# Performance work log

Measured on AMD Instinct MI355X. Metric: run time of the kernel, lower is better.

The kernel has to match this reference:

```python
import jax, jax.numpy as jnp
import numpy as np

B = 4; S_L = 512; WIN = 256; SCH = 3; CCH = 128; F = 8; P = 4; RNN = 128; FC = 256
L1 = (WIN - F + 1) // P          # after conv1 + pool1
L2 = (L1 - F + 1) // P           # after conv2 + pool2
D1 = L2 * CCH                    # flattened conv feature dim fed to GRU


def _conv1d(x, w, b):
    # x: (N, W, Cin), w: (F, Cin, Cout), VALID, stride 1 (matches keras Conv1D)
    return jax.lax.conv_general_dilated(x, w, (1,), 'VALID', dimension_numbers=('NWC', 'WIO', 'NWC')) + b


def _maxpool(x, p):
    return jax.lax.reduce_window(x, -jnp.inf, jax.lax.max, (1, p, 1), (1, p, 1), 'VALID')


def _gru(x, h0, mask, W, U, b):
    # keras GRU v2 (reset_after=True). b[0]=input bias, b[1]=recurrent bias.
    # Masked steps carry state through (keras semantics: output==state for GRU).
    u = U.shape[0]
    xg = x @ W + b[0]  # (B, T, 3u) precomputed input projections
    br = b[1]

    def step(h, inp):
        xt, mt = inp  # (B, 3u), (B,)
        rg = h @ U + br
        z = jax.nn.sigmoid(xt[:, :u] + rg[:, :u])
        r = jax.nn.sigmoid(xt[:, u:2 * u] + rg[:, u:2 * u])
        hh = jnp.tanh(xt[:, 2 * u:] + r * rg[:, 2 * u:])
        hn = z * h + (1.0 - z) * hh
        hn = jnp.where(mt[:, None], hn, h)
        return hn, hn

    _, ys = jax.lax.scan(step, h0, (jnp.swapaxes(xg, 0, 1), jnp.swapaxes(mask, 0, 1)))
    return jnp.swapaxes(ys, 0, 1)  # (B, T, u)


def _bidir(x, m, hf, hb, Wf, Uf, bf, Wb, Ub, bb):
    # Bidirectional(merge='concat'); backward layer sees reversed inputs+mask,
    # its output is reversed back to align with time (keras behaviour).
    yf = _gru(x, hf, m, Wf, Uf, bf)
    yb = _gru(x[:, ::-1], hb, m[:, ::-1], Wb, Ub, bb)[:, ::-1]
    return jnp.concatenate([yf, yb], axis=-1)


def _forward(x, state1_f, state1_b, state2_f, state2_b,
             conv1_w, conv1_b, conv2_w, conv2_b,
             g1f_W, g1f_U, g1f_b, g1b_W, g1b_U, g1b_b,
             g2f_W, g2f_U, g2f_b, g2b_W, g2b_U, g2b_b,
             d1_w, d1_b, d2_w, d2_b, d3_w, d3_b, m):
    bsz = x.shape[0]
    h = x.reshape(bsz * S_L, WIN, SCH)
    h = _maxpool(jax.nn.leaky_relu(_conv1d(h, conv1_w, conv1_b), 0.2), P)
    h = _maxpool(jax.nn.leaky_relu(_conv1d(h, conv2_w, conv2_b), 0.2), P)
    h = h.reshape(bsz, S_L, D1)
    h = _bidir(h, m, state1_f, state1_b, g1f_W, g1f_U, g1f_b, g1b_W, g1b_U, g1b_b)
    h = _bidir(h, m, state2_f, state2_b, g2f_W, g2f_U, g2f_b, g2b_W, g2b_U, g2b_b)
    # keras layers.Attention(use_scale=False): dot-product self attention,
    # key mask -> -1e9 on scores, query mask -> zero outputs.
    scores = jnp.einsum('btd,bsd->bts', h, h)
    scores = jnp.where(m[:, None, :], scores, -1e9)
    h = jnp.einsum('bts,bsd->btd', jax.nn.softmax(scores, axis=-1), h)
    h = h * m[:, :, None].astype(h.dtype)
    h = jax.nn.leaky_relu(h @ d1_w + d1_b, 0.2)   # dropout is identity at inference
    h = jax.nn.leaky_relu(h @ d2_w + d2_b, 0.2)
    return (h @ d3_w + d3_b)[..., 0]              # squeeze -> (B, s_l)


def setup_inputs() -> dict:
    key = jax.random.key(0)
    ks = jax.random.split(key, 32)
    g = lambda k, s: jax.random.normal(k, s, jnp.float32) * 0.05
    inp = {}
    inp['x'] = jax.random.normal(ks[0], (B, S_L, WIN, SCH), jnp.float32)
    inp['m'] = jax.random.randint(ks[1], (B, S_L), 0, 2) > 0
    inp['state1_f'] = jax.random.uniform(ks[2], (B, RNN), jnp.float32, -1.0, 1.0)
    inp['state1_b'] = jax.random.uniform(ks[3], (B, RNN), jnp.float32, -1.0, 1.0)
    inp['state2_f'] = jax.random.uniform(ks[4], (B, RNN), jnp.float32, -1.0, 1.0)
    inp['state2_b'] = jax.random.uniform(ks[5], (B, RNN), jnp.float32, -1.0, 1.0)
    inp['conv1_w'] = g(ks[6], (F, SCH, CCH)); inp['conv1_b'] = jnp.zeros((CCH,), jnp.float32)
    inp['conv2_w'] = g(ks[7], (F, CCH, CCH)); inp['conv2_b'] = jnp.zeros((CCH,), jnp.float32)
    i = 8
    for nm, din in (('g1f', D1), ('g1b', D1), ('g2f', 2 * RNN), ('g2b', 2 * RNN)):
        inp[nm + '_W'] = g(ks[i], (din, 3 * RNN))
        inp[nm + '_U'] = g(ks[i + 1], (RNN, 3 * RNN))
        inp[nm + '_b'] = jnp.zeros((2, 3 * RNN), jnp.float32)
        i += 2
    inp['d1_w'] = g(ks[i], (2 * RNN, FC)); inp['d1_b'] = jnp.zeros((FC,), jnp.float32)
    inp['d2_w'] = g(ks[i + 1], (FC, FC)); inp['d2_b'] = jnp.zeros((FC,), jnp.float32)
    inp['d3_w'] = g(ks[i + 2], (FC, 1)); inp['d3_b'] = jnp.zeros((1,), jnp.float32)
    return inp


def reference(x, m, state1_f, state1_b, state2_f, state2_b,
              conv1_w, conv1_b, conv2_w, conv2_b,
              g1f_W, g1f_U, g1f_b, g1b_W, g1b_U, g1b_b,
              g2f_W, g2f_U, g2f_b, g2b_W, g2b_U, g2b_b,
              d1_w, d1_b, d2_w, d2_b, d3_w, d3_b):
    return _forward(x, state1_f, state1_b, state2_f, state2_b,
                    conv1_w, conv1_b, conv2_w, conv2_b,
                    g1f_W, g1f_U, g1f_b, g1b_W, g1b_U, g1b_b,
                    g2f_W, g2f_U, g2f_b, g2b_W, g2b_U, g2b_b,
                    d1_w, d1_b, d2_w, d2_b, d3_w, d3_b, m)
```

## Files before the change

### kernel.cpp

```cpp
#include <hip/hip_runtime.h>

#define LRELU(v) ((v) > 0.f ? (v) : 0.2f * (v))

typedef float f32x4 __attribute__((ext_vector_type(4)));
typedef __bf16 bf16x8 __attribute__((ext_vector_type(8)));
typedef unsigned short ushort8v __attribute__((ext_vector_type(8)));
typedef unsigned int u32x2 __attribute__((ext_vector_type(2)));

__device__ __forceinline__ unsigned short f2bf(float f) {
    unsigned int u = __float_as_uint(f);
    u += 0x7fffu + ((u >> 16) & 1u);
    return (unsigned short)(u >> 16);
}
__device__ __forceinline__ float bf2f(unsigned short h) {
    return __uint_as_float(((unsigned int)h) << 16);
}
__device__ __forceinline__ float sigmoid_fast(float x) {
    float e = __builtin_amdgcn_exp2f(-x * 1.442695041f);
    return __builtin_amdgcn_rcpf(1.f + e);
}
__device__ __forceinline__ float tanh_fast(float x) {
    float e = __builtin_amdgcn_exp2f(x * 2.885390082f);
    return 1.f - 2.f * __builtin_amdgcn_rcpf(e + 1.f);
}
__device__ __forceinline__ float dpp_add_xor1(float v) {
    int r = __builtin_amdgcn_mov_dpp(__float_as_int(v), 0xB1, 0xF, 0xF, true);
    return v + __int_as_float(r);
}
__device__ __forceinline__ float dpp_add_xor2(float v) {
    int r = __builtin_amdgcn_mov_dpp(__float_as_int(v), 0x4E, 0xF, 0xF, true);
    return v + __int_as_float(r);
}

__global__ void mask_decode_kernel(const unsigned int* __restrict__ mraw,
                                   int* __restrict__ mi) {
    __shared__ int is_u8;
    if (threadIdx.x == 0) {
        int u8 = 0;
        for (int i = 0; i < 512; i++) {
            if (mraw[i] > 1u) { u8 = 1; break; }
        }
        is_u8 = u8;
    }
    __syncthreads();
    if (is_u8) {
        const unsigned char* b8 = (const unsigned char*)mraw;
        for (int i = threadIdx.x; i < 2048; i += blockDim.x) mi[i] = b8[i] ? 1 : 0;
    } else {
        for (int i = threadIdx.x; i < 2048; i += blockDim.x) mi[i] = mraw[i] ? 1 : 0;
    }
}

__global__ __launch_bounds__(256) void prepack_w2(const float* __restrict__ w2,
                                                  unsigned short* __restrict__ bth,
                                                  unsigned short* __restrict__ btl) {
    int idx = blockIdx.x * 256 + threadIdx.x;
    int c = idx >> 10, k = idx & 1023;
    float v = w2[k * 128 + c];
    unsigned short hi = f2bf(v);
    unsigned short lo = f2bf(v - bf2f(hi));
    bth[(long)c * 1024 + k] = hi;
    btl[(long)c * 1024 + k] = lo;
}

__global__ __launch_bounds__(256) void prepack_wt(const float* __restrict__ W,
                                                  unsigned short* __restrict__ h,
                                                  unsigned short* __restrict__ l,
                                                  int K, int N) {
    long idx = (long)blockIdx.x * 256 + threadIdx.x;
    if (idx >= (long)K * N) return;
    int n = (int)(idx / K), k = (int)(idx % K);
    float v = W[(long)k * N + n];
    unsigned short hi = f2bf(v);
    unsigned short lo = f2bf(v - bf2f(hi));
    h[idx] = hi;
    l[idx] = lo;
}

__global__ __launch_bounds__(256) void prepack_ugru(const float* __restrict__ U,
                                                    float* __restrict__ up) {
    int widx = blockIdx.x * 256 + threadIdx.x;
    if (widx >= 49152) return;
    int quad = widx >> 11;
    int rem = widx & 2047;
    int t = rem >> 2, i = rem & 3;
    int g = quad >> 3, q = quad & 7;
    int c = t >> 2, kq = t & 3;
    up[widx] = U[(long)(kq * 32 + q * 4 + i) * 384 + g * 128 + c];
}

__global__ __launch_bounds__(256) void conv_kernel(
    const float* __restrict__ x, const float* __restrict__ w1,
    const float* __restrict__ b1, const unsigned short* __restrict__ bth,
    const unsigned short* __restrict__ btl, const float* __restrict__ b2,
    unsigned short* __restrict__ feat_h, unsigned short* __restrict__ feat_l) {
    __shared__ float xs[3][256];
    __shared__ __align__(16) unsigned short p1h[72 * 128];
    __shared__ __align__(16) unsigned short p1l[72 * 128];
    long s = blockIdx.x;
    int tid = threadIdx.x;
    const float* xp = x + s * 768;
    for (int i = tid; i < 768; i += 256) xs[i % 3][i / 3] = xp[i];
    for (int i = tid; i < 10 * 128; i += 256) {
        p1h[62 * 128 + i] = 0;
        p1l[62 * 128 + i] = 0;
    }
    __syncthreads();

    {
        int ch = tid & 127;
        int half = tid >> 7;
        float w1r[24];
#pragma unroll
        for (int fc = 0; fc < 24; fc++) w1r[fc] = w1[fc * 128 + ch];
        float bias1 = b1[ch];
        for (int po = half; po < 62; po += 2) {
            int p0 = po * 4;
            float a0 = bias1, a1 = bias1, a2 = bias1, a3 = bias1;
#pragma unroll
            for (int c = 0; c < 3; c++) {
                float xv[11];
#pragma unroll
                for (int q = 0; q < 11; q++) xv[q] = xs[c][p0 + q];
#pragma unroll
                for (int f = 0; f < 8; f++) {
                    float w = w1r[f * 3 + c];
                    a0 = fmaf(xv[f + 0], w, a0);
                    a1 = fmaf(xv[f + 1], w, a1);
                    a2 = fmaf(xv[f + 2], w, a2);
                    a3 = fmaf(xv[f + 3], w, a3);
                }
            }
            float m01 = fmaxf(LRELU(a0), LRELU(a1));
            float m23 = fmaxf(LRELU(a2), LRELU(a3));
            float v = fmaxf(m01, m23);
            unsigned short hi = f2bf(v);
            unsigned short lo = f2bf(v - bf2f(hi));
            int cs = ch ^ ((po & 7) << 3);
            p1h[po * 128 + cs] = hi;
            p1l[po * 128 + cs] = lo;
        }
    }
    __syncthreads();

    const int l = tid & 63, w = tid >> 6;
    const int r = l & 15, g = l >> 4;
    f32x4 acc[4][2];
    const f32x4 zz = {0.f, 0.f, 0.f, 0.f};
#pragma unroll
    for (int m = 0; m < 4; m++) {
        acc[m][0] = zz;
        acc[m][1] = zz;
    }
#pragma unroll 2
    for (int ks = 0; ks < 32; ks++) {
        const int f = ks >> 2;
        const int cin0 = ((ks & 3) << 5) + (g << 3);
        bf16x8 bh[2], bl[2];
#pragma unroll
        for (int n = 0; n < 2; n++) {
            const int c = ((w << 1) + n) * 16 + r;
            const long bo = (long)c * 1024 + (ks << 5) + (g << 3);
            bh[n] = __builtin_bit_cast(bf16x8, *(const ushort8v*)(bth + bo));
            bl[n] = __builtin_bit_cast(bf16x8, *(const ushort8v*)(btl + bo));
        }
        bf16x8 ah[4], al[4];
#pragma unroll
        for (int m = 0; m < 4; m++) {
            const int row = m * 16 + r + f;
            const int col = cin0 ^ ((row & 7) << 3);
            const int off = row * 128 + col;
            ah[m] = __builtin_bit_cast(bf16x8, *(const ushort8v*)(p1h + off));
            al[m] = __builtin_bit_cast(bf16x8, *(const ushort8v*)(p1l + off));
        }
#pragma unroll
        for (int m = 0; m < 4; m++) {
#pragma unroll
            for (int n = 0; n < 2; n++) {
                acc[m][n] = __builtin_amdgcn_mfma_f32_16x16x32_bf16(ah[m], bh[n], acc[m][n], 0, 0, 0);
                acc[m][n] = __builtin_amdgcn_mfma_f32_16x16x32_bf16(ah[m], bl[n], acc[m][n], 0, 0, 0);
                acc[m][n] = __builtin_amdgcn_mfma_f32_16x16x32_bf16(al[m], bh[n], acc[m][n], 0, 0, 0);
            }
        }
    }
#pragma unroll
    for (int m = 0; m < 4; m++) {
        const int j = m * 4 + g;
        if (j < 13) {
#pragma unroll
            for (int n = 0; n < 2; n++) {
                const int ch = ((w << 1) + n) * 16 + r;
                const float bias = b2[ch];
                float v0 = LRELU(acc[m][n].x + bias);
                float v1 = LRELU(acc[m][n].y + bias);
                float v2 = LRELU(acc[m][n].z + bias);
                float v3 = LRELU(acc[m][n].w + bias);
                float v = fmaxf(fmaxf(v0, v1), fmaxf(v2, v3));
                unsigned short hi = f2bf(v);
                feat_h[s * 1664 + j * 128 + ch] = hi;
                feat_l[s * 1664 + j * 128 + ch] = f2bf(v - bf2f(hi));
            }
        }
    }
}

template <int MASK>
__global__ __launch_bounds__(256) void gemm_bf16v2(
    const unsigned short* __restrict__ Agh, const unsigned short* __restrict__ Agl,
    const unsigned short* __restrict__ Bth, const unsigned short* __restrict__ Btl,
    const float* __restrict__ bias, const int* __restrict__ mask,
    float* __restrict__ C, long sAz, long sBz, long sCz,
    int M, int N, int K) {
    const int bz = blockIdx.z;
    Agh += (long)bz * sAz;
    Agl += (long)bz * sAz;
    Bth += (long)bz * sBz;
    Btl += (long)bz * sBz;
    C += (long)bz * sCz;
    __shared__ __align__(16) unsigned short Ahs[64 * 32];
    __shared__ __align__(16) unsigned short Als[64 * 32];
    const int tid = threadIdx.x;
    const int w = tid >> 6, l = tid & 63, r = l & 15, g = l >> 4;
    const int m0 = blockIdx.y * 64, n0 = blockIdx.x * 64;
    const int col = n0 + w * 16 + r;
    const int srow = tid >> 2, sgq = tid & 3;
    f32x4 acc[4];
    const f32x4 zz = {0.f, 0.f, 0.f, 0.f};
#pragma unroll
    for (int m = 0; m < 4; m++) acc[m] = zz;

    const long abase = (long)(m0 + srow) * K + ((sgq ^ (srow & 3)) << 3);
    const long bbase = (long)col * K + g * 8;
    ushort8v bhc = *(const ushort8v*)(Bth + bbase);
    ushort8v blc = *(const ushort8v*)(Btl + bbase);

    for (int k0 = 0; k0 < K; k0 += 32) {
        __syncthreads();
        __builtin_amdgcn_global_load_lds(
            (const __attribute__((address_space(1))) void*)(Agh + abase + k0),
            (__attribute__((address_space(3))) void*)&Ahs[tid * 8], 16, 0, 0);
        __builtin_amdgcn_global_load_lds(
            (const __attribute__((address_space(1))) void*)(Agl + abase + k0),
            (__attribute__((address_space(3))) void*)&Als[tid * 8], 16, 0, 0);
        ushort8v nbh, nbl;
        if (k0 + 32 < K) {
            nbh = *(const ushort8v*)(Bth + bbase + k0 + 32);
            nbl = *(const ushort8v*)(Btl + bbase + k0 + 32);
        }
        __syncthreads();
        bf16x8 bh = __builtin_bit_cast(bf16x8, bhc);
        bf16x8 bl = __builtin_bit_cast(bf16x8, blc);
#pragma unroll
        for (int m = 0; m < 4; m++) {
            const int arow = m * 16 + r;
            const int aoff = arow * 32 + ((g ^ (arow & 3)) << 3);
            bf16x8 ah = __builtin_bit_cast(bf16x8, *(const ushort8v*)(Ahs + aoff));
            bf16x8 al = __builtin_bit_cast(bf16x8, *(const ushort8v*)(Als + aoff));
            acc[m] = __builtin_amdgcn_mfma_f32_16x16x32_bf16(ah, bh, acc[m], 0, 0, 0);
            acc[m] = __builtin_amdgcn_mfma_f32_16x16x32_bf16(ah, bl, acc[m], 0, 0, 0);
            acc[m] = __builtin_amdgcn_mfma_f32_16x16x32_bf16(al, bh, acc[m], 0, 0, 0);
        }
        bhc = nbh;
        blc = nbl;
    }
    float bv = 0.f;
    int mk = 1;
    if (MASK == 0) {
        bv = bias ? bias[col] : 0.f;
    } else {
        mk = mask[bz * 512 + col];
    }
#pragma unroll
    for (int m = 0; m < 4; m++) {
#pragma unroll
        for (int q = 0; q < 4; q++) {
            const int row = m0 + m * 16 + g * 4 + q;
            float v = acc[m][q] + bv;
            if (MASK == 1) v = mk ? v : -1e9f;
            C[(long)row * N + col] = v;
        }
    }
}

template <int ACT>
__global__ __launch_bounds__(256) void gemm_nn(
    const float* __restrict__ A, long sA, const float* __restrict__ B, long sB,
    const float* __restrict__ bias, const int* __restrict__ qmask,
    float* __restrict__ C, long sC, int M, int N, int K) {
    int bz = blockIdx.z;
    A += (long)bz * sA;
    B += (long)bz * sB;
    C += (long)bz * sC;
    __shared__ __align__(16) float As[16][68];
    __shared__ __align__(16) float Bs[16][68];
    int tid = threadIdx.x;
    int tm = tid >> 4, tn = tid & 15;
    int m0 = blockIdx.y * 64, n0 = blockIdx.x * 64;
    int la_m = tid & 63, la_k = (tid >> 6) * 4;
    int lb_k = tid >> 4, lb_n = (tid & 15) * 4;
    float acc[4][4] = {};
    for (int k0 = 0; k0 < K; k0 += 16) {
        float4 av = *(const float4*)&A[(long)(m0 + la_m) * K + k0 + la_k];
        float4 bv = *(const float4*)&B[(long)(k0 + lb_k) * N + n0 + lb_n];
        As[la_k + 0][la_m] = av.x;
        As[la_k + 1][la_m] = av.y;
        As[la_k + 2][la_m] = av.z;
        As[la_k + 3][la_m] = av.w;
        *(float4*)&Bs[lb_k][lb_n] = bv;
        __syncthreads();
#pragma unroll
        for (int k = 0; k < 16; k++) {
            float4 a4 = *(const float4*)&As[k][tm * 4];
            float4 b4 = *(const float4*)&Bs[k][tn * 4];
            float aa[4] = {a4.x, a4.y, a4.z, a4.w};
            float bb[4] = {b4.x, b4.y, b4.z, b4.w};
#pragma unroll
            for (int i = 0; i < 4; i++)
#pragma unroll
                for (int j = 0; j < 4; j++) acc[i][j] = fmaf(aa[i], bb[j], acc[i][j]);
        }
        __syncthreads();
    }
#pragma unroll
    for (int i = 0; i < 4; i++) {
        int row = m0 + tm * 4 + i;
        float msc = qmask ? (float)qmask[(long)bz * M + row] : 1.f;
#pragma unroll
        for (int j = 0; j < 4; j++) {
            int col = n0 + tn * 4 + j;
            float v = acc[i][j] + (bias ? bias[col] : 0.f);
            if (ACT == 1) v = LRELU(v);
            C[(long)row * N + col] = v * msc;
        }
    }
}

__global__ __launch_bounds__(256) void softmax_kernel(float* __restrict__ S) {
    long row = blockIdx.x;
    float* p = S + row * 512;
    int tid = threadIdx.x;
    __shared__ float red[8];
    float v0 = p[tid], v1 = p[tid + 256];
    float mx = fmaxf(v0, v1);
#pragma unroll
    for (int off = 32; off; off >>= 1) mx = fmaxf(mx, __shfl_down(mx, off));
    if ((tid & 63) == 0) red[tid >> 6] = mx;
    __syncthreads();
    mx = fmaxf(fmaxf(red[0], red[1]), fmaxf(red[2], red[3]));
    float e0 = expf(v0 - mx), e1 = expf(v1 - mx);
    float sm = e0 + e1;
#pragma unroll
    for (int off = 32; off; off >>= 1) sm += __shfl_down(sm, off);
    if ((tid & 63) == 0) red[4 + (tid >> 6)] = sm;
    __syncthreads();
    float inv = 1.f / (red[4] + red[5] + red[6] + red[7]);
    p[tid] = e0 * inv;
    p[tid + 256] = e1 * inv;
}

#define D4(a0, a1, hv, uv)           \
    a0 = fmaf(hv.x, uv.x, a0);       \
    a1 = fmaf(hv.y, uv.y, a1);       \
    a0 = fmaf(hv.z, uv.z, a0);       \
    a1 = fmaf(hv.w, uv.w, a1);

template <int WF32>
__global__ __launch_bounds__(512, 2) void gru_kernel(
    const float* __restrict__ xgf, const float* __restrict__ xgb,
    const float* __restrict__ Upf, const float* __restrict__ Upb,
    const float* __restrict__ brf, const float* __restrict__ brb,
    const float* __restrict__ h0f, const float* __restrict__ h0b,
    const int* __restrict__ mask, float* __restrict__ out,
    unsigned short* __restrict__ outh, unsigned short* __restrict__ outl) {
    int b = blockIdx.x & 3;
    int dir = blockIdx.x >> 2;
    const float* __restrict__ xg = dir ? xgb : xgf;
    const float* __restrict__ Up = dir ? Upb : Upf;
    const float* __restrict__ br = dir ? brb : brf;
    const float* __restrict__ h0 = dir ? h0b : h0f;
    const int tid = threadIdx.x;
    const int c = tid >> 2;
    const int kq = tid & 3;

    __shared__ __align__(16) float xs[2][16 * 384];
    __shared__ __align__(16) float hsh[2][144];
    __shared__ __align__(16) unsigned int histp[16][128];
    __shared__ __align__(16) float histf[16][128];
    __shared__ unsigned long long mwords[8];

    auto stage = [&](int cc, int bufi) {
#pragma unroll
        for (int i = 0; i < 3; i++) {
            int g = i * 512 + tid;
            int j = g / 96;
            int col = (g - j * 96) * 4;
            int ts = cc * 16 + j;
            int t = dir ? (511 - ts) : ts;
            const float* src = xg + ((long)(b * 512 + t)) * 384 + col;
            __builtin_amdgcn_global_load_lds(
                (const __attribute__((address_space(1))) void*)src,
                (__attribute__((address_space(3))) void*)&xs[bufi][g * 4], 16, 0, 0);
        }
    };
    stage(0, 0);

    const float* ub = Up + (tid << 2);
    f32x4 uz0 = *(const f32x4*)(ub + 0 * 2048);
    f32x4 uz1 = *(const f32x4*)(ub + 1 * 2048);
    f32x4 uz2 = *(const f32x4*)(ub + 2 * 2048);
    f32x4 uz3 = *(const f32x4*)(ub + 3 * 2048);
    f32x4 uz4 = *(const f32x4*)(ub + 4 * 2048);
    f32x4 uz5 = *(const f32x4*)(ub + 5 * 2048);
    f32x4 uz6 = *(const f32x4*)(ub + 6 * 2048);
    f32x4 uz7 = *(const f32x4*)(ub + 7 * 2048);
    f32x4 ur0 = *(const f32x4*)(ub + 8 * 2048);
    f32x4 ur1 = *(const f32x4*)(ub + 9 * 2048);
    f32x4 ur2 = *(const f32x4*)(ub + 10 * 2048);
    f32x4 ur3 = *(const f32x4*)(ub + 11 * 2048);
    f32x4 ur4 = *(const f32x4*)(ub + 12 * 2048);
    f32x4 ur5 = *(const f32x4*)(ub + 13 * 2048);
    f32x4 ur6 = *(const f32x4*)(ub + 14 * 2048);
    f32x4 ur7 = *(const f32x4*)(ub + 15 * 2048);
    f32x4 uh0 = *(const f32x4*)(ub + 16 * 2048);
    f32x4 uh1 = *(const f32x4*)(ub + 17 * 2048);
    f32x4 uh2 = *(const f32x4*)(ub + 18 * 2048);
    f32x4 uh3 = *(const f32x4*)(ub + 19 * 2048);
    f32x4 uh4 = *(const f32x4*)(ub + 20 * 2048);
    f32x4 uh5 = *(const f32x4*)(ub + 21 * 2048);
    f32x4 uh6 = *(const f32x4*)(ub + 22 * 2048);
    f32x4 uh7 = *(const f32x4*)(ub + 23 * 2048);

    float br3[3];
#pragma unroll
    for (int g = 0; g < 3; g++) br3[g] = br[g * 128 + c];

    float hreg = h0[b * 128 + c];
    if (kq == 0) hsh[0][c + (c >> 5) * 4] = hreg;
    if (tid < 64) {
#pragma unroll
        for (int w = 0; w < 8; w++) {
            int idx = w * 64 + tid;
            int t = dir ? (511 - idx) : idx;
            unsigned long long bm = __ballot(mask[b * 512 + t] != 0);
            if (tid == 0) mwords[w] = bm;
        }
    }
    asm volatile("s_waitcnt lgkmcnt(0)" ::: "memory");
    __builtin_amdgcn_s_barrier();

    int cur = 0;
    for (int cc = 0; cc < 32; cc++) {
        asm volatile("s_waitcnt vmcnt(0)" ::: "memory");
        if (cc < 31) stage(cc + 1, (cc + 1) & 1);
        __builtin_amdgcn_s_barrier();
        const float* xb = xs[cc & 1];
        unsigned mwbits = (unsigned)((mwords[cc >> 2] >> ((cc & 3) * 16)) & 0xffffull);
#pragma unroll 1
        for (int jj = 0; jj < 16; jj++) {
            if ((mwbits >> jj) & 1) {
                const float* hp = &hsh[cur][kq * 36];
                float4 h0v = *(const float4*)(hp + 0);
                float4 h1v = *(const float4*)(hp + 4);
                float4 h2v = *(const float4*)(hp + 8);
                float4 h3v = *(const float4*)(hp + 12);
                float4 h4v = *(const float4*)(hp + 16);
                float4 h5v = *(const float4*)(hp + 20);
                float4 h6v = *(const float4*)(hp + 24);
                float4 h7v = *(const float4*)(hp + 28);
                float az0 = 0.f, az1 = 0.f, ar0 = 0.f, ar1 = 0.f, ah0 = 0.f, ah1 = 0.f;
                D4(az0, az1, h0v, uz0) D4(az0, az1, h1v, uz1)
                D4(az0, az1, h2v, uz2) D4(az0, az1, h3v, uz3)
                D4(az0, az1, h4v, uz4) D4(az0, az1, h5v, uz5)
                D4(az0, az1, h6v, uz6) D4(az0, az1, h7v, uz7)
                D4(ar0, ar1, h0v, ur0) D4(ar0, ar1, h1v, ur1)
                D4(ar0, ar1, h2v, ur2) D4(ar0, ar1, h3v, ur3)
                D4(ar0, ar1, h4v, ur4) D4(ar0, ar1, h5v, ur5)
                D4(ar0, ar1, h6v, ur6) D4(ar0, ar1, h7v, ur7)
                D4(ah0, ah1, h0v, uh0) D4(ah0, ah1, h1v, uh1)
                D4(ah0, ah1, h2v, uh2) D4(ah0, ah1, h3v, uh3)
                D4(ah0, ah1, h4v, uh4) D4(ah0, ah1, h5v, uh5)
                D4(ah0, ah1, h6v, uh6) D4(ah0, ah1, h7v, uh7)
                float rgz = dpp_add_xor2(dpp_add_xor1(az0 + az1));
                float rgr = dpp_add_xor2(dpp_add_xor1(ar0 + ar1));
                float rgh = dpp_add_xor2(dpp_add_xor1(ah0 + ah1));
                if (kq == 0) {
                    float xz = xb[jj * 384 + c];
                    float xr = xb[jj * 384 + 128 + c];
                    float xh = xb[jj * 384 + 256 + c];
                    float z = sigmoid_fast(xz + rgz + br3[0]);
                    float r_ = sigmoid_fast(xr + rgr + br3[1]);
                    float hc = tanh_fast(fmaf(r_, rgh + br3[2], xh));
                    float hn = fmaf(z, hreg - hc, hc);
                    hreg = hn;
                    hsh[cur ^ 1][c + (c >> 5) * 4] = hn;
                    if (WF32) histf[jj][c] = hn;
                    unsigned short hh = f2bf(hn);
                    histp[jj][c] = (unsigned)hh |
                                   ((unsigned)f2bf(hn - bf2f(hh)) << 16);
                }
                asm volatile("s_waitcnt lgkmcnt(0)" ::: "memory");
                __builtin_amdgcn_s_barrier();
                cur ^= 1;
            } else {
                if (kq == 0) {
                    if (WF32) histf[jj][c] = hreg;
                    unsigned short hh = f2bf(hreg);
                    histp[jj][c] = (unsigned)hh |
                                   ((unsigned)f2bf(hreg - bf2f(hh)) << 16);
                }
            }
        }
        asm volatile("s_waitcnt lgkmcnt(0)" ::: "memory");
        __builtin_amdgcn_s_barrier();
        {
            int fj = tid >> 5, fc = (tid & 31) << 2;
            int ts2 = cc * 16 + fj;
            int tf = dir ? (511 - ts2) : ts2;
            long ob = ((long)(b * 512 + tf)) * 256 + dir * 128 + fc;
            uint4 hp4 = *(const uint4*)&histp[fj][fc];
            u32x2 ph, pl;
            ph.x = (hp4.x & 0xffffu) | (hp4.y << 16);
            ph.y = (hp4.z & 0xffffu) | (hp4.w << 16);
            pl.x = (hp4.x >> 16) | (hp4.y & 0xffff0000u);
            pl.y = (hp4.z >> 16) | (hp4.w & 0xffff0000u);
            *(u32x2*)(outh + ob) = ph;
            *(u32x2*)(outl + ob) = pl;
            if (WF32) *(float4*)(out + ob) = *(const float4*)&histf[fj][fc];
        }
    }
}

__global__ __launch_bounds__(256) void final_kernel(
    const float* __restrict__ fc2, const float* __restrict__ w,
    const float* __restrict__ b, float* __restrict__ out) {
    int row = blockIdx.x * 4 + (threadIdx.x >> 6);
    int lane = threadIdx.x & 63;
    const float* a = fc2 + (long)row * 256;
    float acc = 0.f;
#pragma unroll
    for (int i = 0; i < 4; i++) acc = fmaf(a[lane + i * 64], w[lane + i * 64], acc);
#pragma unroll
    for (int off = 32; off; off >>= 1) acc += __shfl_down(acc, off);
    if (lane == 0) out[row] = acc + b[0];
}

extern "C" void kernel_launch(void* const* d_in, const int* in_sizes, int n_in,
                              void* d_out, int out_size, void* d_ws,
                              size_t ws_size, hipStream_t stream) {
    const float* x = (const float*)d_in[0];
    const unsigned int* mraw = (const unsigned int*)d_in[1];
    const float* s1f = (const float*)d_in[2];
    const float* s1b = (const float*)d_in[3];
    const float* s2f = (const float*)d_in[4];
    const float* s2b = (const float*)d_in[5];
    const float* c1w = (const float*)d_in[6];
    const float* c1b = (const float*)d_in[7];
    const float* c2w = (const float*)d_in[8];
    const float* c2b = (const float*)d_in[9];
    const float* g1fW = (const float*)d_in[10];
    const float* g1fU = (const float*)d_in[11];
    const float* g1fb = (const float*)d_in[12];
    const float* g1bW = (const float*)d_in[13];
    const float* g1bU = (const float*)d_in[14];
    const float* g1bb = (const float*)d_in[15];
    const float* g2fW = (const float*)d_in[16];
    const float* g2fU = (const float*)d_in[17];
    const float* g2fb = (const float*)d_in[18];
    const float* g2bW = (const float*)d_in[19];
    const float* g2bU = (const float*)d_in[20];
    const float* g2bb = (const float*)d_in[21];
    const float* d1w = (const float*)d_in[22];
    const float* d1b = (const float*)d_in[23];
    const float* d2w = (const float*)d_in[24];
    const float* d2b = (const float*)d_in[25];
    const float* d3w = (const float*)d_in[26];
    const float* d3b = (const float*)d_in[27];
    float* out = (float*)d_out;

    float* ws = (float*)d_ws;
    size_t off = 0;
    auto take = [&](size_t n) {
        float* p = ws + off;
        off += (n + 63) & ~(size_t)63;
        return p;
    };
    int* mask_i = (int*)take(2048);
    unsigned short* feat_h = (unsigned short*)take(2048UL * 1664 / 2);
    unsigned short* feat_l = (unsigned short*)take(2048UL * 1664 / 2);
    float* xg1f = take(2048UL * 384);
    float* xg1b = take(2048UL * 384);
    unsigned short* gru1h = (unsigned short*)take(2048UL * 128);
    unsigned short* gru1l = (unsigned short*)take(2048UL * 128);
    float* xg2f = take(2048UL * 384);
    float* xg2b = take(2048UL * 384);
    float* gru2 = take(2048UL * 256);
    unsigned short* gru2h = (unsigned short*)take(2048UL * 128);
    unsigned short* gru2l = (unsigned short*)take(2048UL * 128);
    float* sc = take(4UL * 512 * 512);
    float* attn = take(2048UL * 256);
    float* fc1 = take(2048UL * 256);
    float* fc2 = take(2048UL * 256);
    unsigned short* bth = (unsigned short*)take(65536);
    unsigned short* btl = (unsigned short*)take(65536);
    unsigned short* wt1fh = (unsigned short*)take(319488);
    unsigned short* wt1fl = (unsigned short*)take(319488);
    unsigned short* wt1bh = (unsigned short*)take(319488);
    unsigned short* wt1bl = (unsigned short*)take(319488);
    unsigned short* wt2fh = (unsigned short*)take(49152);
    unsigned short* wt2fl = (unsigned short*)take(49152);
    unsigned short* wt2bh = (unsigned short*)take(49152);
    unsigned short* wt2bl = (unsigned short*)take(49152);
    float* up1f = take(49152);
    float* up1b = take(49152);
    float* up2f = take(49152);
    float* up2b = take(49152);

    mask_decode_kernel<<<1, 256, 0, stream>>>(mraw, mask_i);
    prepack_w2<<<512, 256, 0, stream>>>(c2w, bth, btl);
    prepack_wt<<<2496, 256, 0, stream>>>(g1fW, wt1fh, wt1fl, 1664, 384);
    prepack_wt<<<2496, 256, 0, stream>>>(g1bW, wt1bh, wt1bl, 1664, 384);
    prepack_wt<<<384, 256, 0, stream>>>(g2fW, wt2fh, wt2fl, 256, 384);
    prepack_wt<<<384, 256, 0, stream>>>(g2bW, wt2bh, wt2bl, 256, 384);
    prepack_ugru<<<192, 256, 0, stream>>>(g1fU, up1f);
    prepack_ugru<<<192, 256, 0, stream>>>(g1bU, up1b);
    prepack_ugru<<<192, 256, 0, stream>>>(g2fU, up2f);
    prepack_ugru<<<192, 256, 0, stream>>>(g2bU, up2b);
    conv_kernel<<<2048, 256, 0, stream>>>(x, c1w, c1b, bth, btl, c2b, feat_h, feat_l);

    gemm_bf16v2<0><<<dim3(6, 32, 1), 256, 0, stream>>>(
        feat_h, feat_l, wt1fh, wt1fl, g1fb, nullptr, xg1f, 0, 0, 0, 2048, 384, 1664);
    gemm_bf16v2<0><<<dim3(6, 32, 1), 256, 0, stream>>>(
        feat_h, feat_l, wt1bh, wt1bl, g1bb, nullptr, xg1b, 0, 0, 0, 2048, 384, 1664);
    gru_kernel<0><<<8, 512, 0, stream>>>(xg1f, xg1b, up1f, up1b, g1fb + 384,
                                         g1bb + 384, s1f, s1b, mask_i, nullptr,
                                         gru1h, gru1l);

    gemm_bf16v2<0><<<dim3(6, 32, 1), 256, 0, stream>>>(
        gru1h, gru1l, wt2fh, wt2fl, g2fb, nullptr, xg2f, 0, 0, 0, 2048, 384, 256);
    gemm_bf16v2<0><<<dim3(6, 32, 1), 256, 0, stream>>>(
        gru1h, gru1l, wt2bh, wt2bl, g2bb, nullptr, xg2b, 0, 0, 0, 2048, 384, 256);
    gru_kernel<1><<<8, 512, 0, stream>>>(xg2f, xg2b, up2f, up2b, g2fb + 384,
                                         g2bb + 384, s2f, s2b, mask_i, gru2,
                                         gru2h, gru2l);

    gemm_bf16v2<1><<<dim3(8, 8, 4), 256, 0, stream>>>(
        gru2h, gru2l, gru2h, gru2l, nullptr, mask_i, sc,
        512L * 256, 512L * 256, 512L * 512, 512, 512, 256);
    softmax_kernel<<<2048, 256, 0, stream>>>(sc);
    gemm_nn<0><<<dim3(4, 8, 4), 256, 0, stream>>>(sc, 512L * 512, gru2, 512L * 256,
                                                  nullptr, mask_i, attn, 512L * 256,
                                                  512, 256, 512);

    gemm_nn<1><<<dim3(4, 32, 1), 256, 0, stream>>>(attn, 0, d1w, 0, d1b, nullptr,
                                                   fc1, 0, 2048, 256, 256);
    gemm_nn<1><<<dim3(4, 32, 1), 256, 0, stream>>>(fc1, 0, d2w, 0, d2b, nullptr,
                                                   fc2, 0, 2048, 256, 256);
    final_kernel<<<512, 256, 0, stream>>>(fc2, d3w, d3b, out);
}
```

Baseline: 765.9 us.

## Merge prepack launches, batch fwd/bwd projection GEMMs, double-buffer GEMM LDS

Folds the ten prepack and mask-decode kernels into one multi-role launch. The two forward/backward input-projection GEMMs per GRU layer become one launch with grid z=2. The bf16 split GEMMs now double-buffer their A tiles in LDS, issuing the next tile's async global-to-LDS load before the MFMA work with one barrier per step. This cuts launch overhead and exposed load latency, at the cost of twice the LDS per block and a specialized scores kernel.

```diff
diff --git a/kernel.cpp b/kernel.cpp
--- a/kernel.cpp
+++ b/kernel.cpp
@@ -32,61 +32,78 @@
     return v + __int_as_float(r);
 }
 
-__global__ void mask_decode_kernel(const unsigned int* __restrict__ mraw,
-                                   int* __restrict__ mi) {
-    __shared__ int is_u8;
-    if (threadIdx.x == 0) {
-        int u8 = 0;
-        for (int i = 0; i < 512; i++) {
-            if (mraw[i] > 1u) { u8 = 1; break; }
-        }
-        is_u8 = u8;
-    }
-    __syncthreads();
-    if (is_u8) {
-        const unsigned char* b8 = (const unsigned char*)mraw;
-        for (int i = threadIdx.x; i < 2048; i += blockDim.x) mi[i] = b8[i] ? 1 : 0;
-    } else {
-        for (int i = threadIdx.x; i < 2048; i += blockDim.x) mi[i] = mraw[i] ? 1 : 0;
-    }
-}
-
-__global__ __launch_bounds__(256) void prepack_w2(const float* __restrict__ w2,
-                                                  unsigned short* __restrict__ bth,
-                                                  unsigned short* __restrict__ btl) {
-    int idx = blockIdx.x * 256 + threadIdx.x;
-    int c = idx >> 10, k = idx & 1023;
-    float v = w2[k * 128 + c];
-    unsigned short hi = f2bf(v);
-    unsigned short lo = f2bf(v - bf2f(hi));
-    bth[(long)c * 1024 + k] = hi;
-    btl[(long)c * 1024 + k] = lo;
-}
-
-__global__ __launch_bounds__(256) void prepack_wt(const float* __restrict__ W,
-                                                  unsigned short* __restrict__ h,
-                                                  unsigned short* __restrict__ l,
-                                                  int K, int N) {
-    long idx = (long)blockIdx.x * 256 + threadIdx.x;
-    if (idx >= (long)K * N) return;
+__device__ __forceinline__ void wtpack(const float* __restrict__ W,
+                                       unsigned short* __restrict__ h,
+                                       unsigned short* __restrict__ l, int K,
+                                       int N, long idx) {
     int n = (int)(idx / K), k = (int)(idx % K);
     float v = W[(long)k * N + n];
     unsigned short hi = f2bf(v);
-    unsigned short lo = f2bf(v - bf2f(hi));
     h[idx] = hi;
-    l[idx] = lo;
-}
-
-__global__ __launch_bounds__(256) void prepack_ugru(const float* __restrict__ U,
-                                                    float* __restrict__ up) {
-    int widx = blockIdx.x * 256 + threadIdx.x;
-    if (widx >= 49152) return;
+    l[idx] = f2bf(v - bf2f(hi));
+}
+__device__ __forceinline__ void ugpack(const float* __restrict__ U,
+                                       float* __restrict__ up, int widx) {
     int quad = widx >> 11;
     int rem = widx & 2047;
     int t = rem >> 2, i = rem & 3;
     int g = quad >> 3, q = quad & 7;
     int c = t >> 2, kq = t & 3;
     up[widx] = U[(long)(kq * 32 + q * 4 + i) * 384 + g * 128 + c];
+}
+
+__global__ __launch_bounds__(256) void prepack_all(
+    const float* __restrict__ w2, unsigned short* __restrict__ bth,
+    unsigned short* __restrict__ btl, const float* __restrict__ g1fW,
+    unsigned short* __restrict__ wt1fh, unsigned short* __restrict__ wt1fl,
+    const float* __restrict__ g1bW, unsigned short* __restrict__ wt1bh,
+    unsigned short* __restrict__ wt1bl, const float* __restrict__ g2fW,
+    unsigned short* __restrict__ wt2fh, unsigned short* __restrict__ wt2fl,
+    const float* __restrict__ g2bW, unsigned short* __restrict__ wt2bh,
+    unsigned short* __restrict__ wt2bl, const float* __restrict__ g1fU,
+    float* __restrict__ up1f, const float* __restrict__ g1bU,
+    float* __restrict__ up1b, const float* __restrict__ g2fU,
+    float* __restrict__ up2f, const float* __restrict__ g2bU,
+    float* __restrict__ up2b, const unsigned int* __restrict__ mraw,
+    int* __restrict__ mi) {
+    const int bid = blockIdx.x, tid = threadIdx.x;
+    if (bid < 512) {
+        int idx = bid * 256 + tid;
+        int c = idx >> 10, k = idx & 1023;
+        float v = w2[k * 128 + c];
+        unsigned short hi = f2bf(v);
+        bth[(long)c * 1024 + k] = hi;
+        btl[(long)c * 1024 + k] = f2bf(v - bf2f(hi));
+    } else if (bid < 3008) {
+        wtpack(g1fW, wt1fh, wt1fl, 1664, 384, (long)(bid - 512) * 256 + tid);
+    } else if (bid < 5504) {
+        wtpack(g1bW, wt1bh, wt1bl, 1664, 384, (long)(bid - 3008) * 256 + tid);
+    } else if (bid < 5888) {
+        wtpack(g2fW, wt2fh, wt2fl, 256, 384, (long)(bid - 5504) * 256 + tid);
+    } else if (bid < 6272) {
+        wtpack(g2bW, wt2bh, wt2bl, 256, 384, (long)(bid - 5888) * 256 + tid);
+    } else if (bid < 6464) {
+        ugpack(g1fU, up1f, (bid - 6272) * 256 + tid);
+    } else if (bid < 6656) {
+        ugpack(g1bU, up1b, (bid - 6464) * 256 + tid);
+    } else if (bid < 6848) {
+        ugpack(g2fU, up2f, (bid - 6656) * 256 + tid);
+    } else if (bid < 7040) {
+        ugpack(g2bU, up2b, (bid - 6848) * 256 + tid);
+    } else {
+        __shared__ int flag;
+        if (tid == 0) flag = 0;
+        __syncthreads();
+        unsigned a = mraw[tid * 2], bb = mraw[tid * 2 + 1];
+        if (a > 1u || bb > 1u) flag = 1;
+        __syncthreads();
+        if (flag) {
+            const unsigned char* b8 = (const unsigned char*)mraw;
+            for (int i = tid; i < 2048; i += 256) mi[i] = b8[i] ? 1 : 0;
+        } else {
+            for (int i = tid; i < 2048; i += 256) mi[i] = mraw[i] ? 1 : 0;
+        }
+    }
 }
 
 __global__ __launch_bounds__(256) void conv_kernel(
@@ -204,58 +221,61 @@
     }
 }
 
-template <int MASK>
-__global__ __launch_bounds__(256) void gemm_bf16v2(
+__global__ __launch_bounds__(256) void gemm_proj(
     const unsigned short* __restrict__ Agh, const unsigned short* __restrict__ Agl,
-    const unsigned short* __restrict__ Bth, const unsigned short* __restrict__ Btl,
-    const float* __restrict__ bias, const int* __restrict__ mask,
-    float* __restrict__ C, long sAz, long sBz, long sCz,
-    int M, int N, int K) {
-    const int bz = blockIdx.z;
-    Agh += (long)bz * sAz;
-    Agl += (long)bz * sAz;
-    Bth += (long)bz * sBz;
-    Btl += (long)bz * sBz;
-    C += (long)bz * sCz;
-    __shared__ __align__(16) unsigned short Ahs[64 * 32];
-    __shared__ __align__(16) unsigned short Als[64 * 32];
+    const unsigned short* __restrict__ B0h, const unsigned short* __restrict__ B0l,
+    const unsigned short* __restrict__ B1h, const unsigned short* __restrict__ B1l,
+    const float* __restrict__ bias0, const float* __restrict__ bias1,
+    float* __restrict__ C0, float* __restrict__ C1, int M, int N, int K) {
+    const int z = blockIdx.z;
+    const unsigned short* __restrict__ Bth = z ? B1h : B0h;
+    const unsigned short* __restrict__ Btl = z ? B1l : B0l;
+    const float* __restrict__ bias = z ? bias1 : bias0;
+    float* __restrict__ C = z ? C1 : C0;
+    __shared__ __align__(16) unsigned short Ahs[2][64 * 32];
+    __shared__ __align__(16) unsigned short Als[2][64 * 32];
     const int tid = threadIdx.x;
     const int w = tid >> 6, l = tid & 63, r = l & 15, g = l >> 4;
     const int m0 = blockIdx.y * 64, n0 = blockIdx.x * 64;
     const int col = n0 + w * 16 + r;
     const int srow = tid >> 2, sgq = tid & 3;
     f32x4 acc[4];
-    const f32x4 zz = {0.f, 0.f, 0.f, 0.f};
-#pragma unroll
-    for (int m = 0; m < 4; m++) acc[m] = zz;
+    const f32x4 zzv = {0.f, 0.f, 0.f, 0.f};
+#pragma unroll
+    for (int m = 0; m < 4; m++) acc[m] = zzv;
 
     const long abase = (long)(m0 + srow) * K + ((sgq ^ (srow & 3)) << 3);
+    auto stage = [&](int k0, int buf) {
+        __builtin_amdgcn_global_load_lds(
+            (const __attribute__((address_space(1))) void*)(Agh + abase + k0),
+            (__attribute__((address_space(3))) void*)&Ahs[buf][tid * 8], 16, 0, 0);
+        __builtin_amdgcn_global_load_lds(
+            (const __attribute__((address_space(1))) void*)(Agl + abase + k0),
+            (__attribute__((address_space(3))) void*)&Als[buf][tid * 8], 16, 0, 0);
+    };
+    stage(0, 0);
     const long bbase = (long)col * K + g * 8;
     ushort8v bhc = *(const ushort8v*)(Bth + bbase);
     ushort8v blc = *(const ushort8v*)(Btl + bbase);
 
     for (int k0 = 0; k0 < K; k0 += 32) {
-        __syncthreads();
-        __builtin_amdgcn_global_load_lds(
-            (const __attribute__((address_space(1))) void*)(Agh + abase + k0),
-            (__attribute__((address_space(3))) void*)&Ahs[tid * 8], 16, 0, 0);
-        __builtin_amdgcn_global_load_lds(
-            (const __attribute__((address_space(1))) void*)(Agl + abase + k0),
-            (__attribute__((address_space(3))) void*)&Als[tid * 8], 16, 0, 0);
+        const int buf = (k0 >> 5) & 1;
+        asm volatile("s_waitcnt vmcnt(0)" ::: "memory");
+        __builtin_amdgcn_s_barrier();
         ushort8v nbh, nbl;
         if (k0 + 32 < K) {
+            stage(k0 + 32, buf ^ 1);
             nbh = *(const ushort8v*)(Bth + bbase + k0 + 32);
             nbl = *(const ushort8v*)(Btl + bbase + k0 + 32);
         }
-        __syncthreads();
         bf16x8 bh = __builtin_bit_cast(bf16x8, bhc);
         bf16x8 bl = __builtin_bit_cast(bf16x8, blc);
 #pragma unroll
         for (int m = 0; m < 4; m++) {
             const int arow = m * 16 + r;
             const int aoff = arow * 32 + ((g ^ (arow & 3)) << 3);
-            bf16x8 ah = __builtin_bit_cast(bf16x8, *(const ushort8v*)(Ahs + aoff));
-            bf16x8 al = __builtin_bit_cast(bf16x8, *(const ushort8v*)(Als + aoff));
+            bf16x8 ah = __builtin_bit_cast(bf16x8, *(const ushort8v*)(&Ahs[buf][aoff]));
+            bf16x8 al = __builtin_bit_cast(bf16x8, *(const ushort8v*)(&Als[buf][aoff]));
             acc[m] = __builtin_amdgcn_mfma_f32_16x16x32_bf16(ah, bh, acc[m], 0, 0, 0);
             acc[m] = __builtin_amdgcn_mfma_f32_16x16x32_bf16(ah, bl, acc[m], 0, 0, 0);
             acc[m] = __builtin_amdgcn_mfma_f32_16x16x32_bf16(al, bh, acc[m], 0, 0, 0);
@@ -263,21 +283,84 @@
         bhc = nbh;
         blc = nbl;
     }
-    float bv = 0.f;
-    int mk = 1;
-    if (MASK == 0) {
-        bv = bias ? bias[col] : 0.f;
-    } else {
-        mk = mask[bz * 512 + col];
-    }
+    const float bv = bias[col];
 #pragma unroll
     for (int m = 0; m < 4; m++) {
 #pragma unroll
         for (int q = 0; q < 4; q++) {
             const int row = m0 + m * 16 + g * 4 + q;
-            float v = acc[m][q] + bv;
-            if (MASK == 1) v = mk ? v : -1e9f;
-            C[(long)row * N + col] = v;
+            C[(long)row * N + col] = acc[m][q] + bv;
+        }
+    }
+}
+
+__global__ __launch_bounds__(256) void gemm_scores(
+    const unsigned short* __restrict__ Hh, const unsigned short* __restrict__ Hl,
+    const int* __restrict__ mask, float* __restrict__ S) {
+    const int bz = blockIdx.z;
+    const unsigned short* __restrict__ Agh = Hh + (long)bz * 512 * 256;
+    const unsigned short* __restrict__ Agl = Hl + (long)bz * 512 * 256;
+    float* __restrict__ C = S + (long)bz * 512 * 512;
+    const int K = 256, N = 512;
+    __shared__ __align__(16) unsigned short Ahs[2][64 * 32];
+    __shared__ __align__(16) unsigned short Als[2][64 * 32];
+    const int tid = threadIdx.x;
+    const int w = tid >> 6, l = tid & 63, r = l & 15, g = l >> 4;
+    const int m0 = blockIdx.y * 64, n0 = blockIdx.x * 64;
+    const int col = n0 + w * 16 + r;
+    const int srow = tid >> 2, sgq = tid & 3;
+    f32x4 acc[4];
+    const f32x4 zzv = {0.f, 0.f, 0.f, 0.f};
+#pragma unroll
+    for (int m = 0; m < 4; m++) acc[m] = zzv;
+
+    const long abase = (long)(m0 + srow) * K + ((sgq ^ (srow & 3)) << 3);
+    auto stage = [&](int k0, int buf) {
+        __builtin_amdgcn_global_load_lds(
+            (const __attribute__((address_space(1))) void*)(Agh + abase + k0),
+            (__attribute__((address_space(3))) void*)&Ahs[buf][tid * 8], 16, 0, 0);
+        __builtin_amdgcn_global_load_lds(
+            (const __attribute__((address_space(1))) void*)(Agl + abase + k0),
+            (__attribute__((address_space(3))) void*)&Als[buf][tid * 8], 16, 0, 0);
+    };
+    stage(0, 0);
+    const long bbase = (long)col * K + g * 8;
+    ushort8v bhc = *(const ushort8v*)(Agh + bbase);
+    ushort8v blc = *(const ushort8v*)(Agl + bbase);
+
+    for (int k0 = 0; k0 < K; k0 += 32) {
+        const int buf = (k0 >> 5) & 1;
+        asm volatile("s_waitcnt vmcnt(0)" ::: "memory");
+        __builtin_amdgcn_s_barrier();
+        ushort8v nbh, nbl;
+        if (k0 + 32 < K) {
+            stage(k0 + 32, buf ^ 1);
+            nbh = *(const ushort8v*)(Agh + bbase + k0 + 32);
+            nbl = *(const ushort8v*)(Agl + bbase + k0 + 32);
+        }
+        bf16x8 bh = __builtin_bit_cast(bf16x8, bhc);
+        bf16x8 bl = __builtin_bit_cast(bf16x8, blc);
+#pragma unroll
+        for (int m = 0; m < 4; m++) {
+            const int arow = m * 16 + r;
+            const int aoff = arow * 32 + ((g ^ (arow & 3)) << 3);
+            bf16x8 ah = __builtin_bit_cast(bf16x8, *(const ushort8v*)(&Ahs[buf][aoff]));
+            bf16x8 al = __builtin_bit_cast(bf16x8, *(const ushort8v*)(&Als[buf][aoff]));
+            acc[m] = __builtin_amdgcn_mfma_f32_16x16x32_bf16(ah, bh, acc[m], 0, 0, 0);
+            acc[m] = __builtin_amdgcn_mfma_f32_16x16x32_bf16(ah, bl, acc[m], 0, 0, 0);
+            acc[m] = __builtin_amdgcn_mfma_f32_16x16x32_bf16(al, bh, acc[m], 0, 0, 0);
+        }
+        bhc = nbh;
+        blc = nbl;
+    }
+    const int mk = mask[bz * 512 + col];
+#pragma unroll
+    for (int m = 0; m < 4; m++) {
+#pragma unroll
+        for (int q = 0; q < 4; q++) {
+            const int row = m0 + m * 16 + g * 4 + q;
+            float v = acc[m][q];
+            C[(long)row * N + col] = mk ? v : -1e9f;
         }
     }
 }
@@ -615,37 +698,27 @@
     float* up2f = take(49152);
     float* up2b = take(49152);
 
-    mask_decode_kernel<<<1, 256, 0, stream>>>(mraw, mask_i);
-    prepack_w2<<<512, 256, 0, stream>>>(c2w, bth, btl);
-    prepack_wt<<<2496, 256, 0, stream>>>(g1fW, wt1fh, wt1fl, 1664, 384);
-    prepack_wt<<<2496, 256, 0, stream>>>(g1bW, wt1bh, wt1bl, 1664, 384);
-    prepack_wt<<<384, 256, 0, stream>>>(g2fW, wt2fh, wt2fl, 256, 384);
-    prepack_wt<<<384, 256, 0, stream>>>(g2bW, wt2bh, wt2bl, 256, 384);
-    prepack_ugru<<<192, 256, 0, stream>>>(g1fU, up1f);
-    prepack_ugru<<<192, 256, 0, stream>>>(g1bU, up1b);
-    prepack_ugru<<<192, 256, 0, stream>>>(g2fU, up2f);
-    prepack_ugru<<<192, 256, 0, stream>>>(g2bU, up2b);
+    prepack_all<<<7041, 256, 0, stream>>>(
+        c2w, bth, btl, g1fW, wt1fh, wt1fl, g1bW, wt1bh, wt1bl, g2fW, wt2fh,
+        wt2fl, g2bW, wt2bh, wt2bl, g1fU, up1f, g1bU, up1b, g2fU, up2f, g2bU,
+        up2b, mraw, mask_i);
     conv_kernel<<<2048, 256, 0, stream>>>(x, c1w, c1b, bth, btl, c2b, feat_h, feat_l);
 
-    gemm_bf16v2<0><<<dim3(6, 32, 1), 256, 0, stream>>>(
-        feat_h, feat_l, wt1fh, wt1fl, g1fb, nullptr, xg1f, 0, 0, 0, 2048, 384, 1664);
-    gemm_bf16v2<0><<<dim3(6, 32, 1), 256, 0, stream>>>(
-        feat_h, feat_l, wt1bh, wt1bl, g1bb, nullptr, xg1b, 0, 0, 0, 2048, 384, 1664);
+    gemm_proj<<<dim3(6, 32, 2), 256, 0, stream>>>(
+        feat_h, feat_l, wt1fh, wt1fl, wt1bh, wt1bl, g1fb, g1bb, xg1f, xg1b,
+        2048, 384, 1664);
     gru_kernel<0><<<8, 512, 0, stream>>>(xg1f, xg1b, up1f, up1b, g1fb + 384,
                                          g1bb + 384, s1f, s1b, mask_i, nullptr,
                                          gru1h, gru1l);
 
-    gemm_bf16v2<0><<<dim3(6, 32, 1), 256, 0, stream>>>(
-        gru1h, gru1l, wt2fh, wt2fl, g2fb, nullptr, xg2f, 0, 0, 0, 2048, 384, 256);
-    gemm_bf16v2<0><<<dim3(6, 32, 1), 256, 0, stream>>>(
-        gru1h, gru1l, wt2bh, wt2bl, g2bb, nullptr, xg2b, 0, 0, 0, 2048, 384, 256);
+    gemm_proj<<<dim3(6, 32, 2), 256, 0, stream>>>(
+        gru1h, gru1l, wt2fh, wt2fl, wt2bh, wt2bl, g2fb, g2bb, xg2f, xg2b,
+        2048, 384, 256);
     gru_kernel<1><<<8, 512, 0, stream>>>(xg2f, xg2b, up2f, up2b, g2fb + 384,
                                          g2bb + 384, s2f, s2b, mask_i, gru2,
                                          gru2h, gru2l);
 
-    gemm_bf16v2<1><<<dim3(8, 8, 4), 256, 0, stream>>>(
-        gru2h, gru2l, gru2h, gru2l, nullptr, mask_i, sc,
-        512L * 256, 512L * 256, 512L * 512, 512, 512, 256);
+    gemm_scores<<<dim3(8, 8, 4), 256, 0, stream>>>(gru2h, gru2l, mask_i, sc);
     softmax_kernel<<<2048, 256, 0, stream>>>(sc);
     gemm_nn<0><<<dim3(4, 8, 4), 256, 0, stream>>>(sc, 512L * 512, gru2, 512L * 256,
                                                   nullptr, mask_i, attn, 512L * 256,
```

After: 669.1 us. -12.6%, faster.
